# Performance work log

Measured on AMD Instinct MI355X. Metric: run time of the kernel, lower is better.

## Reference

```python
import jax, jax.numpy as jnp
import numpy as np

# Module constants (from init_kwargs / defaults)
OUT_SIZE = (4, 32, 32)      # (Z, X, Y) grid
REAL_SIZE = (3.0, 25.0, 25.0)
SCALE = 1.4
THRESHOLD = 0.5
D_ELEMS = np.array([0.74 * SCALE, 0.528 * SCALE], dtype=np.float32)  # per-element match/NMS radius (O, H)


def _transform(x):
    """(B, X, Y, Z, 4*E) -> coords (B, E, N, 3), conf (B, E, N); N = Z*X*Y."""
    B, X, Y, Z, L = x.shape
    E = L // 4
    v = x.reshape(B, X, Y, Z, E, 4).transpose(0, 4, 3, 1, 2, 5)   # (B,E,Z,X,Y,4)
    v = v[..., jnp.array([2, 0, 1, 3])]                            # reorder last dim
    Zs, Xs, Ys = OUT_SIZE
    ind = jnp.stack(jnp.meshgrid(jnp.arange(Zs), jnp.arange(Xs), jnp.arange(Ys), indexing='ij'),
                    axis=-1).astype(x.dtype)                       # (Z,X,Y,3) == torch nonzero of ones
    expand = jnp.array([r / o for o, r in zip(OUT_SIZE, REAL_SIZE)], dtype=x.dtype)
    coords = (v[..., :3] + ind) * expand
    conf = v[..., 3]
    N = Zs * Xs * Ys
    return coords.reshape(B, E, N, 3), conf.reshape(B, E, N)


def _sort_by_conf(coords, conf):
    order = jnp.argsort(-conf, axis=-1)
    coords = jnp.take_along_axis(coords, order[..., None], axis=2)
    conf = jnp.take_along_axis(conf, order, axis=-1)
    return coords, conf


def _nms(pts, valid, d):
    """Greedy sequential NMS on one (N,3) point set. Point b is suppressed if any
    still-selected earlier point a<b lies within distance d. Invalid points never suppress."""
    N = pts.shape[0]
    d2 = jnp.sum((pts[:, None, :] - pts[None, :, :]) ** 2, axis=-1)   # (N,N)
    ar = jnp.arange(N)
    M = (d2 < d * d) & valid[:, None] & valid[None, :] & (ar[:, None] < ar[None, :])

    def body(b, sel):
        return sel.at[b].set(~jnp.any(sel & M[:, b]))

    sel = jax.lax.fori_loop(0, N, body, jnp.ones((N,), bool))
    return sel & valid


def _match(P, T, keepP, keepT, d):
    """Greedy row-major bipartite matching: each pred (in order) grabs the first
    still-unmatched target within distance d. Returns (TP, FP, FN) masks."""
    N = P.shape[0]
    d2 = jnp.sum((P[:, None, :] - T[None, :, :]) ** 2, axis=-1)      # (N,N)
    D = (d2 < d * d) & keepP[:, None] & keepT[None, :]

    def body(a, carry):
        selP, selT = carry
        avail = D[a] & ~selT
        has = jnp.any(avail)
        j = jnp.argmax(avail)                    # first available target index
        selT = selT.at[j].set(selT[j] | has)
        selP = selP.at[a].set(has)
        return (selP, selT)

    selP, selT = jax.lax.fori_loop(0, N, body,
                                   (jnp.zeros((N,), bool), jnp.zeros((N,), bool)))
    return selP, keepP & ~selP, keepT & ~selT    # TP, FP, FN masks


def setup_inputs() -> dict:
    key = jax.random.key(0)
    k1, k2 = jax.random.split(key)
    B = 4
    predictions = jax.random.normal(k1, (B, 32, 32, 4, 8), dtype=jnp.float32)
    targets = jax.random.normal(k2, (B, 32, 32, 4, 8), dtype=jnp.float32)
    return {"predictions": predictions, "targets": targets}


def reference(predictions, targets):
    Pc, Pconf = _sort_by_conf(*_transform(predictions))   # (B,E,N,3), (B,E,N)
    Tc, Tconf = _sort_by_conf(*_transform(targets))
    validP = Pconf > THRESHOLD
    validT = Tconf > THRESHOLD
    d = jnp.asarray(D_ELEMS)                               # (E,)

    nms_be = jax.vmap(jax.vmap(_nms, in_axes=(0, 0, 0)), in_axes=(0, 0, None))
    keepP = nms_be(Pc, validP, d)                          # (B,E,N) bool
    keepT = nms_be(Tc, validT, d)

    match_be = jax.vmap(jax.vmap(_match, in_axes=(0, 0, 0, 0, 0)), in_axes=(0, 0, 0, 0, None))
    tp, fp, fn = match_be(Pc, Tc, keepP, keepT, d)         # (B,E,N) bool each

    # sorted real-space points, NMS-kept masks, and TP/FP/FN masks (fixed-shape
    # equivalents of the torch module's filtered P/T/TP/FP/FN lists)
    return Pc, Tc, keepP, keepT, tp, fp, fn
```

## Files before the change

### kernel.cpp

```cpp
#include <hip/hip_runtime.h>
#include <hip/hip_bf16.h>

#pragma clang fp contract(off)

#define NPTS 4096
#define BE   8
#define COORD_SZ (BE * NPTS * 3)
#define MASK_SZ  (BE * NPTS)
#define OFF_PC   0
#define OFF_TC   (COORD_SZ)
#define OFF_KP   (2 * COORD_SZ)
#define OFF_KT   (2 * COORD_SZ + MASK_SZ)
#define OFF_TP   (2 * COORD_SZ + 2 * MASK_SZ)
#define OFF_FP   (2 * COORD_SZ + 3 * MASK_SZ)
#define OFF_FN   (2 * COORD_SZ + 4 * MASK_SZ)

#define VCAP 1664
#define NW   26

#define WS_KEYS_OFF  0ull
#define WS_V_OFF     524288ull
#define WS_KEEP_OFF  524352ull
#define WS_PP_OFF    528448ull
#define WS_PT_OFF    6066240ull
#define WS_NEED      8835136ull

typedef unsigned long long u64;

__device__ __forceinline__ float get_dd(int e) {
    const float d0 = (float)(0.74 * 1.4);
    const float d1 = (float)(0.528 * 1.4);
    float d = (e == 0) ? d0 : d1;
    return d * d;
}

__global__ __launch_bounds__(1024)
void sort_kernel(const float* __restrict__ pred,
                 const float* __restrict__ targ,
                 float* __restrict__ out,
                 int* __restrict__ Vcnt) {
    __shared__ u64 bufA[NPTS], bufB[NPTS];
    __shared__ unsigned int hist[1024];
    __shared__ unsigned int offarr[1024];
    __shared__ int wsum[16];
    __shared__ int vtot;
    const int s = blockIdx.x;
    const int arr = s & 1, be = s >> 1;
    const int b = be >> 1, e = be & 1;
    const float* __restrict__ src = arr ? targ : pred;
    const int t = threadIdx.x;
    const int lane = t & 63, wv = t >> 6;

    if (t == 0) vtot = 0;
    for (int n = t; n < NPTS; n += 1024) {
        int z = n >> 10, r = n & 1023, x = r >> 5, y = r & 31;
        int base = (((b * 32 + x) * 32 + y) * 4 + z) * 8 + e * 4;
        float conf = src[base + 3];
        unsigned int bits = __float_as_uint(conf);
        unsigned int u = (bits & 0x80000000u) ? ~bits : (bits | 0x80000000u);
        bufA[n] = ((u64)(~u) << 32) | (unsigned int)n;
    }
    __syncthreads();

    const u64 lmask = (1ull << lane) - 1ull;
    for (int k = 0; k < 8; ++k) {
        u64* cur = (k & 1) ? bufB : bufA;
        u64* nxt = (k & 1) ? bufA : bufB;
        const int shift = 32 + (k << 2);
        hist[t] = 0u;
        __syncthreads();

        u64 item[4]; int dg[4]; int rnk[4];
        #pragma unroll
        for (int m = 0; m < 4; ++m) {
            u64 it = cur[m * 1024 + t];
            int d = (int)((it >> shift) & 15);
            u64 eq = ~0ull;
            #pragma unroll
            for (int bb = 0; bb < 4; ++bb) {
                u64 bal = __ballot((d >> bb) & 1);
                eq &= ((d >> bb) & 1) ? bal : ~bal;
            }
            int r = (int)__popcll(eq & lmask);
            if (r == 0) hist[d * 64 + m * 16 + wv] = (unsigned int)__popcll(eq);
            item[m] = it; dg[m] = d; rnk[m] = r;
        }
        __syncthreads();

        {
            int v = (int)hist[t];
            int inc = v;
            #pragma unroll
            for (int dd = 1; dd < 64; dd <<= 1) {
                int x2 = __shfl_up(inc, dd);
                if (lane >= dd) inc += x2;
            }
            if (lane == 63) wsum[wv] = inc;
            __syncthreads();
            if (t < 16) {
                int wtot = wsum[t]; int iv = wtot;
                #pragma unroll
                for (int dd = 1; dd < 16; dd <<= 1) {
                    int x2 = __shfl_up(iv, dd);
                    if (t >= dd) iv += x2;
                }
                wsum[t] = iv - wtot;
            }
            __syncthreads();
            offarr[t] = (unsigned int)(wsum[wv] + (inc - v));
        }
        __syncthreads();

        #pragma unroll
        for (int m = 0; m < 4; ++m) {
            int pos = (int)offarr[dg[m] * 64 + m * 16 + wv] + rnk[m];
            nxt[pos] = item[m];
        }
        __syncthreads();
    }

    int myv = 0;
    for (int p = t; p < NPTS; p += 1024) {
        u64 key = bufA[p];
        int n = (int)(key & 0xFFFFFFFFull);
        myv += ((unsigned int)(key >> 32) < 0x40FFFFFFu) ? 1 : 0;
        int z = n >> 10, rr = n & 1023, x = rr >> 5, y = rr & 31;
        int base = (((b * 32 + x) * 32 + y) * 4 + z) * 8 + e * 4;
        float r0 = src[base + 0], r1 = src[base + 1], r2 = src[base + 2];
        float c0 = (r2 + (float)z) * 0.75f;
        float c1 = (r0 + (float)x) * 0.78125f;
        float c2 = (r1 + (float)y) * 0.78125f;
        float* dst = out + (size_t)arr * COORD_SZ + ((size_t)be * NPTS + p) * 3;
        dst[0] = c0; dst[1] = c1; dst[2] = c2;
    }
    atomicAdd(&vtot, myv);
    __syncthreads();
    if (t == 0) Vcnt[s] = vtot;
}

__global__ __launch_bounds__(256)
void matrix_kernel(const float* __restrict__ out,
                   const int* __restrict__ Vcnt,
                   u64* __restrict__ ws64) {
    __shared__ float4 tcol[VCAP];
    __shared__ float rowc[64][3];
    const int bx = blockIdx.x;
    const int j = bx / 26, c = bx % 26;
    const int t = threadIdx.x;

    int sRow, sCol, e;
    u64* dstBase;
    if (j < 16) {
        sRow = j; sCol = j; e = (j >> 1) & 1;
        dstBase = ws64 + (WS_PP_OFF / 8) + (size_t)j * VCAP * NW;
    } else {
        int be = j - 16;
        sRow = be * 2 + 0; sCol = be * 2 + 1; e = be & 1;
        dstBase = ws64 + (WS_PT_OFF / 8) + (size_t)be * VCAP * NW;
    }
    int Vr = Vcnt[sRow]; if (Vr > VCAP) Vr = VCAP;
    int Vc = Vcnt[sCol]; if (Vc > VCAP) Vc = VCAP;
    const int rb = c * 64;
    if (rb >= Vr) return;
    const float dd = get_dd(e);

    const float* __restrict__ colc = out + (size_t)(sCol & 1) * COORD_SZ + (size_t)(sCol >> 1) * NPTS * 3;
    const float* __restrict__ rowp = out + (size_t)(sRow & 1) * COORD_SZ + (size_t)(sRow >> 1) * NPTS * 3;

    for (int idx = t; idx < Vc * 3; idx += 256) {
        float v = colc[idx];
        int p = idx / 3, k = idx % 3;
        ((float*)&tcol[p])[k] = v;
    }
    for (int idx = t; idx < 192; idx += 256) {
        int i = idx / 3, k = idx % 3;
        if (rb + i < Vr) rowc[i][k] = rowp[(rb + i) * 3 + k];
    }
    __syncthreads();

    const int NWc = (Vc + 63) >> 6;
    const int wlimit = (j < 16) ? (c + 1) : NWc;
    const int i = t & 63;
    const bool rowOK = (rb + i) < Vr;
    if (rowOK) {
        float ax = rowc[i][0], ay = rowc[i][1], az = rowc[i][2];
        u64* dstRow = dstBase + (size_t)(rb + i) * NW;
        for (int w = t >> 6; w < wlimit; w += 4) {
            int jbase = w << 6;
            int jmax = Vc - jbase; if (jmax > 64) jmax = 64;
            u64 m = 0ull;
            for (int jj = 0; jj < jmax; ++jj) {
                float4 tc = tcol[jbase + jj];
                float dx = ax - tc.x, dy = ay - tc.y, dz = az - tc.z;
                float d2 = dx * dx + dy * dy + dz * dz;
                m |= (d2 < dd) ? (1ull << jj) : 0ull;
            }
            dstRow[w] = m;
        }
    }
}

__global__ __launch_bounds__(1024)
void nms_rounds_kernel(float* __restrict__ out,
                       const int* __restrict__ Vcnt,
                       u64* __restrict__ ws64) {
    __shared__ u64 U[NW];
    __shared__ u64 K[NW];
    __shared__ int remaining;
    const int s = blockIdx.x;
    const int arr = s & 1, be = s >> 1;
    const int t = threadIdx.x;
    int V = Vcnt[s]; if (V > VCAP) V = VCAP;
    const u64* __restrict__ Mx = ws64 + (WS_PP_OFF / 8) + (size_t)s * VCAP * NW;

    if (t < NW) {
        int base = t << 6;
        int rem = V - base;
        u64 u = (rem >= 64) ? ~0ull : ((rem > 0) ? ((1ull << rem) - 1ull) : 0ull);
        U[t] = u;
        K[t] = 0ull;
    }
    if (t == 0) remaining = V;
    __syncthreads();

    while (remaining > 0) {
        bool dec0 = false, keep0 = false;
        bool dec1 = false, keep1 = false;

        {
            const int i = t;
            if (i < V && ((U[i >> 6] >> (i & 63)) & 1ull)) {
                const u64* __restrict__ row = Mx + (size_t)i * NW;
                const int wi = i >> 6;
                u64 cu = 0ull, ck = 0ull;
                int w = 0;
                for (; w + 4 <= wi; w += 4) {
                    u64 m0 = row[w], m1 = row[w + 1], m2 = row[w + 2], m3 = row[w + 3];
                    cu |= (m0 & U[w]) | (m1 & U[w + 1]) | (m2 & U[w + 2]) | (m3 & U[w + 3]);
                    ck |= (m0 & K[w]) | (m1 & K[w + 1]) | (m2 & K[w + 2]) | (m3 & K[w + 3]);
                }
                for (; w < wi; ++w) {
                    u64 m = row[w];
                    cu |= m & U[w];
                    ck |= m & K[w];
                }
                u64 low = (1ull << (i & 63)) - 1ull;
                u64 md = row[wi] & low;
                cu |= md & U[wi];
                ck |= md & K[wi];
                if (cu == 0ull) { dec0 = true; keep0 = (ck == 0ull); }
            }
        }
        {
            const int i = t + 1024;
            if (i < V && ((U[i >> 6] >> (i & 63)) & 1ull)) {
                const u64* __restrict__ row = Mx + (size_t)i * NW;
                const int wi = i >> 6;
                u64 cu = 0ull, ck = 0ull;
                int w = 0;
                for (; w + 4 <= wi; w += 4) {
                    u64 m0 = row[w], m1 = row[w + 1], m2 = row[w + 2], m3 = row[w + 3];
                    cu |= (m0 & U[w]) | (m1 & U[w + 1]) | (m2 & U[w + 2]) | (m3 & U[w + 3]);
                    ck |= (m0 & K[w]) | (m1 & K[w + 1]) | (m2 & K[w + 2]) | (m3 & K[w + 3]);
                }
                for (; w < wi; ++w) {
                    u64 m = row[w];
                    cu |= m & U[w];
                    ck |= m & K[w];
                }
                u64 low = (1ull << (i & 63)) - 1ull;
                u64 md = row[wi] & low;
                cu |= md & U[wi];
                ck |= md & K[wi];
                if (cu == 0ull) { dec1 = true; keep1 = (ck == 0ull); }
            }
        }
        __syncthreads();

        int ndec = 0;
        if (dec0) {
            const int i = t;
            atomicAnd(&U[i >> 6], ~(1ull << (i & 63)));
            if (keep0) atomicOr(&K[i >> 6], 1ull << (i & 63));
            ndec++;
        }
        if (dec1) {
            const int i = t + 1024;
            atomicAnd(&U[i >> 6], ~(1ull << (i & 63)));
            if (keep1) atomicOr(&K[i >> 6], 1ull << (i & 63));
            ndec++;
        }
        if (ndec) atomicSub(&remaining, ndec);
        __syncthreads();
    }

    u64* kb = ws64 + (WS_KEEP_OFF / 8) + s * 32;
    if (t < 32) kb[t] = (t < NW) ? K[t] : 0ull;
    const size_t kbase = (arr == 0 ? OFF_KP : OFF_KT) + (size_t)be * NPTS;
    for (int p = t; p < NPTS; p += 1024) {
        bool k = (p < V) && ((K[p >> 6] >> (p & 63)) & 1ull);
        out[kbase + p] = k ? 1.0f : 0.0f;
    }
}

__global__ __launch_bounds__(1024)
void match_resolve_kernel(float* __restrict__ out,
                          const int* __restrict__ Vcnt,
                          u64* __restrict__ ws64) {
    __shared__ u64 rowbuf[2][64][NW + 1];
    __shared__ u64 kPw[NW], kTw[NW], matchedM[NW], fnTs[NW];
    __shared__ unsigned short rowlist[VCAP];
    __shared__ int wp[NW];
    __shared__ int Mcnt;
    __shared__ unsigned int selP32[128];
    const int be = blockIdx.x;
    const int t = threadIdx.x;
    int Vp = Vcnt[be * 2 + 0]; if (Vp > VCAP) Vp = VCAP;
    int Vt = Vcnt[be * 2 + 1]; if (Vt > VCAP) Vt = VCAP;
    const int NWt = (Vt + 63) >> 6;
    const u64* __restrict__ PT = ws64 + (WS_PT_OFF / 8) + (size_t)be * VCAP * NW;

    if (t < NW) {
        kPw[t] = ws64[(WS_KEEP_OFF / 8) + (be * 2 + 0) * 32 + t];
        kTw[t] = ws64[(WS_KEEP_OFF / 8) + (be * 2 + 1) * 32 + t];
        matchedM[t] = 0ull;
    }
    if (t < 128) selP32[t] = 0u;
    __syncthreads();

    if (t < 64) {
        int cP = (t < NW) ? __popcll(kPw[t]) : 0;
        int o = cP;
        for (int d = 1; d < 64; d <<= 1) {
            int v = __shfl_up(o, d);
            if (t >= d) o += v;
        }
        if (t < NW) wp[t] = o - cP;
        if (t == NW - 1) Mcnt = o;
    }
    __syncthreads();
    const int M = Mcnt;
    const int nrch = (M + 63) >> 6;

    for (int a = t; a < Vp; a += 1024) {
        int w = a >> 6, bb = a & 63;
        u64 word = kPw[w];
        if ((word >> bb) & 1ull) {
            int pos = wp[w] + __popcll(word & ((1ull << bb) - 1ull));
            rowlist[pos] = (unsigned short)a;
        }
    }
    __syncthreads();

    auto stage = [&](int rc, int buf, int tbase, int nth) {
        int rcnt = M - (rc << 6); if (rcnt > 64) rcnt = 64;
        for (int idx = tbase; idx < 64 * NW; idx += nth) {
            int i = idx / NW, w = idx - i * NW;
            u64 v = 0ull;
            if (i < rcnt && w < NWt)
                v = PT[(size_t)rowlist[(rc << 6) + i] * NW + w];
            rowbuf[buf][i][w] = v;
        }
    };
    if (nrch > 0) stage(0, 0, t, 1024);
    __syncthreads();

    u64 availTw = (t < NW) ? kTw[t] : 0ull;

    for (int rc = 0; rc < nrch; ++rc) {
        const int buf = rc & 1;
        if (t < 64) {
            u64 matched = 0ull;
            u64 cur[8], nxt[8];
            const bool lw = (t < NWt);
            #pragma unroll
            for (int k = 0; k < 8; ++k) cur[k] = lw ? rowbuf[buf][k][t] : 0ull;
            for (int g = 0; g < 8; ++g) {
                if (g < 7) {
                    #pragma unroll
                    for (int k = 0; k < 8; ++k) nxt[k] = lw ? rowbuf[buf][(g + 1) * 8 + k][t] : 0ull;
                }
                #pragma unroll
                for (int k = 0; k < 8; ++k) {
                    u64 avail = cur[k] & availTw;
                    u64 bal = __ballot(avail != 0ull);
                    if (bal) {
                        matched |= 1ull << (g * 8 + k);
                        if (t == (int)__builtin_ctzll(bal))
                            availTw &= ~(1ull << (int)__builtin_ctzll(avail));
                    }
                }
                #pragma unroll
                for (int k = 0; k < 8; ++k) cur[k] = nxt[k];
            }
            if (t == 0) matchedM[rc] = matched;
        } else if (rc + 1 < nrch) {
            stage(rc + 1, (rc + 1) & 1, t - 64, 960);
        }
        __syncthreads();
    }

    if (t < NW) fnTs[t] = availTw;
    __syncthreads();

    for (int g = t; g < M; g += 1024) {
        if ((matchedM[g >> 6] >> (g & 63)) & 1ull) {
            int a = rowlist[g];
            atomicOr(&selP32[a >> 5], 1u << (a & 31));
        }
    }
    __syncthreads();

    for (int n = t; n < NPTS; n += 1024) {
        int w = n >> 6;
        bool kpb = (w < NW) && ((kPw[w] >> (n & 63)) & 1ull);
        bool tpb = (selP32[n >> 5] >> (n & 31)) & 1u;
        bool fnb = (w < NW) && ((fnTs[w] >> (n & 63)) & 1ull);
        size_t o = (size_t)be * NPTS + n;
        out[OFF_TP + o] = tpb ? 1.0f : 0.0f;
        out[OFF_FP + o] = (kpb && !tpb) ? 1.0f : 0.0f;
        out[OFF_FN + o] = fnb ? 1.0f : 0.0f;
    }
}

#define FVCAP 2048
#define FNWMAX (FVCAP / 64)

__global__ __launch_bounds__(1024)
void sortnms_fallback(const float* __restrict__ pred,
                      const float* __restrict__ targ,
                      float* __restrict__ out,
                      u64* __restrict__ keepbits) {
    __shared__ u64 skey[NPTS];
    __shared__ float px[FVCAP], py[FVCAP], pz[FVCAP];
    __shared__ u64 kept[FNWMAX];
    __shared__ u64 mchunk[64];
    __shared__ int supp[64];
    __shared__ int vcnt;
    const int blk = blockIdx.x;
    const int arr = blk & 1;
    const int be  = blk >> 1;
    const int b = be >> 1, e = be & 1;
    const float* __restrict__ src = arr ? targ : pred;
    const int t = threadIdx.x;
    const float dd = get_dd(e);
    if (t == 0) vcnt = 0;

    for (int n = t; n < NPTS; n += 1024) {
        int z = n >> 10, r = n & 1023, x = r >> 5, y = r & 31;
        int base = (((b * 32 + x) * 32 + y) * 4 + z) * 8 + e * 4;
        float conf = src[base + 3];
        unsigned int bits = __float_as_uint(conf);
        unsigned int u = (bits & 0x80000000u) ? ~bits : (bits | 0x80000000u);
        skey[n] = ((u64)(~u) << 32) | (unsigned int)n;
    }
    __syncthreads();
    for (int k = 2; k <= NPTS; k <<= 1) {
        for (int j = k >> 1; j > 0; j >>= 1) {
            for (int i = t; i < NPTS; i += 1024) {
                int ixj = i ^ j;
                if (ixj > i) {
                    u64 a = skey[i], c = skey[ixj];
                    bool up = ((i & k) == 0);
                    if ((a > c) == up) { skey[i] = c; skey[ixj] = a; }
                }
            }
            __syncthreads();
        }
    }
    int myv = 0;
    for (int p = t; p < NPTS; p += 1024) {
        u64 key = skey[p];
        int n = (int)(key & 0xFFFFFFFFu);
        unsigned int u = ~(unsigned int)(key >> 32);
        myv += (u > 0xBF000000u) ? 1 : 0;
        int z = n >> 10, r = n & 1023, x = r >> 5, y = r & 31;
        int base = (((b * 32 + x) * 32 + y) * 4 + z) * 8 + e * 4;
        float r0 = src[base + 0], r1 = src[base + 1], r2 = src[base + 2];
        float c0 = (r2 + (float)z) * 0.75f;
        float c1 = (r0 + (float)x) * 0.78125f;
        float c2 = (r1 + (float)y) * 0.78125f;
        float* dst = out + (size_t)arr * COORD_SZ + ((size_t)be * NPTS + p) * 3;
        dst[0] = c0; dst[1] = c1; dst[2] = c2;
        if (p < FVCAP) { px[p] = c0; py[p] = c1; pz[p] = c2; }
    }
    atomicAdd(&vcnt, myv);
    if (t < FNWMAX) kept[t] = 0ull;
    __syncthreads();

    int V = vcnt; if (V > FVCAP) V = FVCAP;
    const int nchunks = (V + 63) >> 6;
    for (int c = 0; c < nchunks; ++c) {
        if (t < 64) supp[t] = 0;
        __syncthreads();
        {
            int i = t & 63, s = t >> 6;
            int p = (c << 6) + i;
            if (p < V) {
                float x = px[p], y = py[p], z = pz[p];
                int lim = c << 6;
                bool f = false;
                for (int j = s; j < lim; j += 16) {
                    if ((kept[j >> 6] >> (j & 63)) & 1ull) {
                        float dx = x - px[j], dy = y - py[j], dz = z - pz[j];
                        float d2 = dx * dx + dy * dy + dz * dz;
                        if (d2 < dd) { f = true; break; }
                    }
                }
                if (f) atomicOr(&supp[i], 1);
            }
        }
        __syncthreads();
        if (t < 64) {
            int p = (c << 6) + t;
            u64 m = 0ull;
            if (p < V) {
                float x = px[p], y = py[p], z = pz[p];
                for (int j = 0; j < t; ++j) {
                    int q = (c << 6) + j;
                    float dx = x - px[q], dy = y - py[q], dz = z - pz[q];
                    float d2 = dx * dx + dy * dy + dz * dz;
                    if (d2 < dd) m |= (1ull << j);
                }
            }
            mchunk[t] = m;
        }
        __syncthreads();
        if (t == 0) {
            u64 kw = 0ull;
            int lim = V - (c << 6); if (lim > 64) lim = 64;
            for (int i = 0; i < lim; ++i) {
                bool ki = (supp[i] == 0) && ((mchunk[i] & kw) == 0ull);
                if (ki) kw |= (1ull << i);
            }
            kept[c] = kw;
        }
        __syncthreads();
    }
    const size_t kbase = (arr == 0 ? OFF_KP : OFF_KT) + (size_t)be * NPTS;
    for (int p = t; p < NPTS; p += 1024) {
        bool kb = (p < V) && ((kept[(p >> 6) & (FNWMAX - 1)] >> (p & 63)) & 1ull);
        out[kbase + p] = kb ? 1.0f : 0.0f;
    }
    if (t < 64) keepbits[blk * 64 + t] = (t < FNWMAX) ? kept[t] : 0ull;
}

__global__ __launch_bounds__(1024)
void match_fallback(float* __restrict__ out,
                    const u64* __restrict__ keepbits) {
    __shared__ float tx[FVCAP], ty[FVCAP], tz[FVCAP];
    __shared__ unsigned short tj[FVCAP];
    __shared__ unsigned short aidx[FVCAP];
    __shared__ unsigned short matchPos[FVCAP];
    __shared__ u64 Mask[64][FNWMAX + 1];
    __shared__ u64 kPm[64], kTm[64];
    __shared__ unsigned int selP32[128], selT32[128];
    __shared__ int wpT[64], wpP[64];
    __shared__ int Mcnt2, Kcnt2;
    __shared__ float pcx[64], pcy[64], pcz[64];
    const int be = blockIdx.x;
    const int e = be & 1;
    const int t = threadIdx.x;
    const float dd = get_dd(e);
    const float* __restrict__ Pc = out + OFF_PC + (size_t)be * NPTS * 3;
    const float* __restrict__ Tc = out + OFF_TC + (size_t)be * NPTS * 3;

    if (t < 64) {
        kPm[t] = keepbits[(be * 2 + 0) * 64 + t];
        kTm[t] = keepbits[(be * 2 + 1) * 64 + t];
    }
    if (t < 128) { selP32[t] = 0u; selT32[t] = 0u; }
    __syncthreads();
    if (t < 64) {
        int cT = __popcll(kTm[t]), cP = __popcll(kPm[t]);
        int oT = cT, oP = cP;
        for (int d = 1; d < 64; d <<= 1) {
            int vT = __shfl_up(oT, d);
            int vP = __shfl_up(oP, d);
            if (t >= d) { oT += vT; oP += vP; }
        }
        wpT[t] = oT - cT;
        wpP[t] = oP - cP;
        if (t == 63) {
            Kcnt2 = (oT > FVCAP) ? FVCAP : oT;
            Mcnt2 = (oP > FVCAP) ? FVCAP : oP;
        }
    }
    __syncthreads();
    const int K = Kcnt2, M = Mcnt2;
    for (int n = t; n < NPTS; n += 1024) {
        int w = n >> 6, bb = n & 63;
        u64 bit = 1ull << bb, lowm = bit - 1ull;
        u64 wT = kTm[w], wP = kPm[w];
        if (wT & bit) {
            int pos = wpT[w] + __popcll(wT & lowm);
            if (pos < FVCAP) {
                tx[pos] = Tc[n * 3 + 0];
                ty[pos] = Tc[n * 3 + 1];
                tz[pos] = Tc[n * 3 + 2];
                tj[pos] = (unsigned short)n;
            }
        }
        if (wP & bit) {
            int pos = wpP[w] + __popcll(wP & lowm);
            if (pos < FVCAP) aidx[pos] = (unsigned short)n;
        }
    }
    __syncthreads();

    const int NWc = (K + 63) >> 6;
    const int nchunks = (M + 63) >> 6;
    u64 selTw = 0ull;

    for (int c = 0; c < nchunks; ++c) {
        int cnt = M - (c << 6); if (cnt > 64) cnt = 64;
        if (t < 64 && t < cnt) {
            int a = aidx[(c << 6) + t];
            pcx[t] = Pc[a * 3 + 0];
            pcy[t] = Pc[a * 3 + 1];
            pcz[t] = Pc[a * 3 + 2];
        }
        __syncthreads();
        {
            int i = t & 63, s = t >> 6;
            if (i < cnt) {
                float ax = pcx[i], ay = pcy[i], az = pcz[i];
                for (int w = s; w < NWc; w += 16) {
                    int jmax = K - (w << 6); if (jmax > 64) jmax = 64;
                    int base = w << 6;
                    u64 m = 0ull;
                    for (int jj = 0; jj < jmax; ++jj) {
                        float dx = ax - tx[base + jj];
                        float dy = ay - ty[base + jj];
                        float dz = az - tz[base + jj];
                        float d2 = dx * dx + dy * dy + dz * dz;
                        m |= (d2 < dd) ? (1ull << jj) : 0ull;
                    }
                    Mask[i][w] = m;
                }
            }
        }
        __syncthreads();
        if (t < 64) {
            u64 mnext = (cnt > 0 && t < NWc) ? Mask[0][t] : 0ull;
            for (int i = 0; i < cnt; ++i) {
                u64 mrow = mnext;
                mnext = (i + 1 < cnt && t < NWc) ? Mask[i + 1][t] : 0ull;
                u64 avail = mrow & ~selTw;
                u64 bal = __ballot(avail != 0ull);
                if (bal) {
                    int w0 = (int)__builtin_ctzll(bal);
                    if (t == w0) {
                        int bb = (int)__builtin_ctzll(avail);
                        selTw |= 1ull << bb;
                        matchPos[(c << 6) + i] = (unsigned short)((w0 << 6) + bb);
                    }
                } else if (t == 0) {
                    matchPos[(c << 6) + i] = 0xffffu;
                }
            }
        }
        __syncthreads();
    }
    for (int g = t; g < M; g += 1024) {
        unsigned short pos = matchPos[g];
        if (pos != 0xffffu) {
            int jj = tj[pos];
            int a  = aidx[g];
            atomicOr(&selT32[jj >> 5], 1u << (jj & 31));
            atomicOr(&selP32[a >> 5],  1u << (a & 31));
        }
    }
    __syncthreads();
    for (int n = t; n < NPTS; n += 1024) {
        bool kpb = (kPm[n >> 6] >> (n & 63)) & 1ull;
        bool ktb = (kTm[n >> 6] >> (n & 63)) & 1ull;
        bool tpb = (selP32[n >> 5] >> (n & 31)) & 1u;
        bool stb = (selT32[n >> 5] >> (n & 31)) & 1u;
        size_t o = (size_t)be * NPTS + n;
        out[OFF_TP + o] = tpb ? 1.0f : 0.0f;
        out[OFF_FP + o] = (kpb && !tpb) ? 1.0f : 0.0f;
        out[OFF_FN + o] = (ktb && !stb) ? 1.0f : 0.0f;
    }
}

extern "C" void kernel_launch(void* const* d_in, const int* in_sizes, int n_in,
                              void* d_out, int out_size, void* d_ws, size_t ws_size,
                              hipStream_t stream) {
    const float* pred = (const float*)d_in[0];
    const float* targ = (const float*)d_in[1];
    float* out = (float*)d_out;

    if (ws_size >= WS_NEED) {
        int* Vcnt = (int*)((char*)d_ws + WS_V_OFF);
        u64* ws64 = (u64*)d_ws;

        sort_kernel<<<16, 1024, 0, stream>>>(pred, targ, out, Vcnt);
        matrix_kernel<<<624, 256, 0, stream>>>(out, Vcnt, ws64);
        nms_rounds_kernel<<<16, 1024, 0, stream>>>(out, Vcnt, ws64);
        match_resolve_kernel<<<8, 1024, 0, stream>>>(out, Vcnt, ws64);
    } else {
        u64* keepbits = (u64*)d_ws;
        sortnms_fallback<<<16, 1024, 0, stream>>>(pred, targ, out, keepbits);
        match_fallback<<<8, 1024, 0, stream>>>(out, keepbits);
    }
}
```

Measured before the change: 185.1 us.

## Replace sequential greedy matching with conflict-graph parallel round resolution

The match kernel no longer scans kept predictions one row at a time with a single wavefront. It builds a conflict matrix between kept predictions (pairs within twice the radius can compete for the same target). Each round it resolves every undecided prediction that has no undecided earlier conflicting prediction, all in parallel. This aims to replace the long serial ballot chain with a few parallel rounds. The cost is an O(M^2) distance pass, global-memory conflict rows, and a number of rounds that depends on the data, so it could be slower when conflicts are dense.

```diff
diff --git a/kernel.cpp b/kernel.cpp
--- a/kernel.cpp
+++ b/kernel.cpp
@@ -307,23 +307,24 @@
 void match_resolve_kernel(float* __restrict__ out,
                           const int* __restrict__ Vcnt,
                           u64* __restrict__ ws64) {
-    __shared__ u64 rowbuf[2][64][NW + 1];
-    __shared__ u64 kPw[NW], kTw[NW], matchedM[NW], fnTs[NW];
+    __shared__ float4 pco[VCAP];
     __shared__ unsigned short rowlist[VCAP];
+    __shared__ u64 kPw[NW], kTw[NW];
+    __shared__ u64 Um[NW];
+    __shared__ u64 availT[NW];
     __shared__ int wp[NW];
-    __shared__ int Mcnt;
+    __shared__ int Mcnt, remaining;
     __shared__ unsigned int selP32[128];
     const int be = blockIdx.x;
+    const int e = be & 1;
     const int t = threadIdx.x;
     int Vp = Vcnt[be * 2 + 0]; if (Vp > VCAP) Vp = VCAP;
-    int Vt = Vcnt[be * 2 + 1]; if (Vt > VCAP) Vt = VCAP;
-    const int NWt = (Vt + 63) >> 6;
     const u64* __restrict__ PT = ws64 + (WS_PT_OFF / 8) + (size_t)be * VCAP * NW;
+    u64* __restrict__ C = ws64 + (WS_PP_OFF / 8) + (size_t)(2 * be) * VCAP * NW;
 
     if (t < NW) {
         kPw[t] = ws64[(WS_KEEP_OFF / 8) + (be * 2 + 0) * 32 + t];
         kTw[t] = ws64[(WS_KEEP_OFF / 8) + (be * 2 + 1) * 32 + t];
-        matchedM[t] = 0ull;
     }
     if (t < 128) selP32[t] = 0u;
     __syncthreads();
@@ -340,7 +341,6 @@
     }
     __syncthreads();
     const int M = Mcnt;
-    const int nrch = (M + 63) >> 6;
 
     for (int a = t; a < Vp; a += 1024) {
         int w = a >> 6, bb = a & 63;
@@ -350,72 +350,101 @@
             rowlist[pos] = (unsigned short)a;
         }
     }
-    __syncthreads();
-
-    auto stage = [&](int rc, int buf, int tbase, int nth) {
-        int rcnt = M - (rc << 6); if (rcnt > 64) rcnt = 64;
-        for (int idx = tbase; idx < 64 * NW; idx += nth) {
-            int i = idx / NW, w = idx - i * NW;
-            u64 v = 0ull;
-            if (i < rcnt && w < NWt)
-                v = PT[(size_t)rowlist[(rc << 6) + i] * NW + w];
-            rowbuf[buf][i][w] = v;
-        }
-    };
-    if (nrch > 0) stage(0, 0, t, 1024);
-    __syncthreads();
-
-    u64 availTw = (t < NW) ? kTw[t] : 0ull;
-
-    for (int rc = 0; rc < nrch; ++rc) {
-        const int buf = rc & 1;
-        if (t < 64) {
-            u64 matched = 0ull;
-            u64 cur[8], nxt[8];
-            const bool lw = (t < NWt);
-            #pragma unroll
-            for (int k = 0; k < 8; ++k) cur[k] = lw ? rowbuf[buf][k][t] : 0ull;
-            for (int g = 0; g < 8; ++g) {
-                if (g < 7) {
-                    #pragma unroll
-                    for (int k = 0; k < 8; ++k) nxt[k] = lw ? rowbuf[buf][(g + 1) * 8 + k][t] : 0ull;
-                }
-                #pragma unroll
-                for (int k = 0; k < 8; ++k) {
-                    u64 avail = cur[k] & availTw;
-                    u64 bal = __ballot(avail != 0ull);
-                    if (bal) {
-                        matched |= 1ull << (g * 8 + k);
-                        if (t == (int)__builtin_ctzll(bal))
-                            availTw &= ~(1ull << (int)__builtin_ctzll(avail));
+    if (t < NW) {
+        int base = t << 6;
+        int rem = M - base;
+        Um[t] = (rem >= 64) ? ~0ull : ((rem > 0) ? ((1ull << rem) - 1ull) : 0ull);
+        availT[t] = kTw[t];
+    }
+    if (t == 0) remaining = M;
+    __syncthreads();
+
+    const float* __restrict__ Pco = out + (size_t)be * NPTS * 3;
+    for (int g = t; g < M; g += 1024) {
+        int a = rowlist[g];
+        pco[g] = make_float4(Pco[a * 3 + 0], Pco[a * 3 + 1], Pco[a * 3 + 2], 0.0f);
+    }
+    __syncthreads();
+
+    const float dd4 = 4.0f * get_dd(e) * (1.0f + 1e-5f);
+    for (int half = 0; half < 2; ++half) {
+        int g = t + half * 1024;
+        if (g < M) {
+            float4 pg = pco[g];
+            int wi = g >> 6;
+            u64* crow = C + (size_t)g * NW;
+            for (int w = 0; w <= wi; ++w) {
+                int jmax = (w == wi) ? (g & 63) : 64;
+                int jb = w << 6;
+                u64 m = 0ull;
+                for (int jj = 0; jj < jmax; ++jj) {
+                    float4 ph = pco[jb + jj];
+                    float dx = pg.x - ph.x, dy = pg.y - ph.y, dz = pg.z - ph.z;
+                    float d2 = dx * dx + dy * dy + dz * dz;
+                    m |= (d2 < dd4) ? (1ull << jj) : 0ull;
+                }
+                crow[w] = m;
+            }
+        }
+    }
+    __syncthreads();
+
+    while (remaining > 0) {
+        bool dec0 = false, dec1 = false;
+        int jt0 = -1, jt1 = -1;
+
+        #pragma unroll
+        for (int half = 0; half < 2; ++half) {
+            const int g = t + half * 1024;
+            if (g < M && ((Um[g >> 6] >> (g & 63)) & 1ull)) {
+                const u64* __restrict__ crow = C + (size_t)g * NW;
+                const int wi = g >> 6;
+                u64 cu = 0ull;
+                for (int w = 0; w <= wi; ++w) cu |= crow[w] & Um[w];
+                if (cu == 0ull) {
+                    const u64* __restrict__ prow = PT + (size_t)rowlist[g] * NW;
+                    int jt = -1;
+                    for (int w = NW - 1; w >= 0; --w) {
+                        u64 av = prow[w] & availT[w];
+                        if (av) jt = (w << 6) + (int)__builtin_ctzll(av);
                     }
-                }
-                #pragma unroll
-                for (int k = 0; k < 8; ++k) cur[k] = nxt[k];
-            }
-            if (t == 0) matchedM[rc] = matched;
-        } else if (rc + 1 < nrch) {
-            stage(rc + 1, (rc + 1) & 1, t - 64, 960);
-        }
-        __syncthreads();
-    }
-
-    if (t < NW) fnTs[t] = availTw;
-    __syncthreads();
-
-    for (int g = t; g < M; g += 1024) {
-        if ((matchedM[g >> 6] >> (g & 63)) & 1ull) {
-            int a = rowlist[g];
-            atomicOr(&selP32[a >> 5], 1u << (a & 31));
-        }
-    }
-    __syncthreads();
+                    if (half == 0) { dec0 = true; jt0 = jt; }
+                    else           { dec1 = true; jt1 = jt; }
+                }
+            }
+        }
+        __syncthreads();
+
+        int ndec = 0;
+        if (dec0) {
+            const int g = t;
+            atomicAnd(&Um[g >> 6], ~(1ull << (g & 63)));
+            if (jt0 >= 0) {
+                atomicAnd(&availT[jt0 >> 6], ~(1ull << (jt0 & 63)));
+                int a = rowlist[g];
+                atomicOr(&selP32[a >> 5], 1u << (a & 31));
+            }
+            ndec++;
+        }
+        if (dec1) {
+            const int g = t + 1024;
+            atomicAnd(&Um[g >> 6], ~(1ull << (g & 63)));
+            if (jt1 >= 0) {
+                atomicAnd(&availT[jt1 >> 6], ~(1ull << (jt1 & 63)));
+                int a = rowlist[g];
+                atomicOr(&selP32[a >> 5], 1u << (a & 31));
+            }
+            ndec++;
+        }
+        if (ndec) atomicSub(&remaining, ndec);
+        __syncthreads();
+    }
 
     for (int n = t; n < NPTS; n += 1024) {
         int w = n >> 6;
         bool kpb = (w < NW) && ((kPw[w] >> (n & 63)) & 1ull);
         bool tpb = (selP32[n >> 5] >> (n & 31)) & 1u;
-        bool fnb = (w < NW) && ((fnTs[w] >> (n & 63)) & 1ull);
+        bool fnb = (w < NW) && ((availT[w] >> (n & 63)) & 1ull);
         size_t o = (size_t)be * NPTS + n;
         out[OFF_TP + o] = tpb ? 1.0f : 0.0f;
         out[OFF_FP + o] = (kpb && !tpb) ? 1.0f : 0.0f;
```

Measured after the change: 248.4 us. 1.34x slower.
